# Kernel optimization log

Measured on AMD Instinct MI355X. Metric: run time of the kernel, lower is better.

Reference implementation:

```python
import jax, jax.numpy as jnp
import numpy as np

VOCAB, DIM, B, L, OUT = 100000, 50, 4096, 512, 20

def setup_inputs() -> dict:
    key = jax.random.key(0)
    k1, k2, k3, k4, k5 = jax.random.split(key, 5)
    x = jax.random.randint(k1, (B, L), 0, VOCAB, dtype=jnp.int64)
    lengths = jax.random.randint(k2, (B,), 1, L + 1, dtype=jnp.int64)  # at least 1 token
    emb_table = jax.random.normal(k3, (VOCAB, DIM), dtype=jnp.float32)
    W = jax.random.normal(k4, (OUT, DIM), dtype=jnp.float32) * 0.1
    b = jax.random.normal(k5, (OUT,), dtype=jnp.float32) * 0.1
    return {"x": x, "lengths": lengths, "emb_table": emb_table, "W": W, "b": b}

def reference(x, lengths, emb_table, W, b):
    # embedding gather: [B, L, D]
    emb = emb_table[x]
    # masked mean over the first lengths[i] tokens of each sample
    mask = (jnp.arange(emb.shape[1])[None, :] < lengths[:, None]).astype(emb.dtype)  # [B, L]
    denom = lengths.astype(emb.dtype)[:, None]                                        # [B, 1]
    rep = jnp.einsum('bld,bl->bd', emb, mask) / denom                                 # [B, D]
    rep = jax.nn.relu(rep)
    logits = rep @ W.T + b                                                            # [B, OUT]
    return logits
```

## Files before the change

kernel.cpp:

```cpp
#include <hip/hip_runtime.h>
#include <hip/hip_fp16.h>


#define LMAX    512
#define DIMV    50
#define OUTV    20
#define VOCABSZ 100000
#define RSTRIDE 64
#define NSHARD  8
#define SHROWS  12500
#define BINCAP  576
#define TABBLKS 3126

struct __align__(16) H8 { __half2 h[4]; };

#define OFF_GBIN  (16u << 20)
#define OFF_BOFS  (28u << 20)
#define OFF_PART  (29u << 20)

__device__ inline void accum(float4& a0, float4& a1, const H8& h) {
    float2 f0 = __half22float2(h.h[0]);
    float2 f1 = __half22float2(h.h[1]);
    float2 f2 = __half22float2(h.h[2]);
    float2 f3 = __half22float2(h.h[3]);
    a0.x += f0.x; a0.y += f0.y; a0.z += f1.x; a0.w += f1.y;
    a1.x += f2.x; a1.y += f2.y; a1.z += f3.x; a1.w += f3.y;
}

__global__ __launch_bounds__(256) void prep(
    const float* __restrict__ emb, const int* __restrict__ x,
    const int* __restrict__ lengths, char* __restrict__ ws)
{
    const int tid = threadIdx.x;

    if (blockIdx.x < TABBLKS) {
        __half* tab = (__half*)ws;
        const int t = blockIdx.x * 256 + tid;
        const int r = t >> 3, q = t & 7;
        if (r > VOCABSZ) return;
        float v[8] = {0.f,0.f,0.f,0.f,0.f,0.f,0.f,0.f};
        if (r < VOCABSZ) {
            const float* src = emb + r * DIMV + q * 8;
            if (q < 6) {
                #pragma unroll
                for (int j = 0; j < 8; j += 2) {
                    float2 a = *reinterpret_cast<const float2*>(src + j);
                    v[j] = a.x; v[j + 1] = a.y;
                }
            } else if (q == 6) {
                float2 a = *reinterpret_cast<const float2*>(src);
                v[0] = a.x; v[1] = a.y;
            }
        }
        H8 h;
        h.h[0] = __floats2half2_rn(v[0], v[1]);
        h.h[1] = __floats2half2_rn(v[2], v[3]);
        h.h[2] = __floats2half2_rn(v[4], v[5]);
        h.h[3] = __floats2half2_rn(v[6], v[7]);
        *reinterpret_cast<H8*>(tab + r * RSTRIDE + q * 8) = h;
        return;
    }

    const int b = blockIdx.x - TABBLKS;
    int*  gbin = (int*)(ws + OFF_GBIN);
    int2* bofs = (int2*)(ws + OFF_BOFS);

    __shared__ int sidx[LMAX];
    __shared__ int sbin[BINCAP];
    __shared__ int cnt[NSHARD], pcnt[NSHARD], base[NSHARD], pos[NSHARD];

    if (tid < NSHARD) { cnt[tid] = 0; pos[tid] = 0; }
    __syncthreads();

    const int len = lengths[b];
    #pragma unroll
    for (int i = tid; i < LMAX; i += 256) {
        const int v = x[b * LMAX + i];
        sidx[i] = v;
        if (i < len) atomicAdd(&cnt[v / SHROWS], 1);
    }
    __syncthreads();
    if (tid == 0) {
        int run = 0;
        #pragma unroll
        for (int s = 0; s < NSHARD; ++s) {
            base[s] = run;
            pcnt[s] = (cnt[s] + 7) & ~7;
            run += pcnt[s];
        }
    }
    __syncthreads();
    #pragma unroll
    for (int i = tid; i < LMAX; i += 256) {
        if (i < len) {
            const int v = sidx[i];
            const int s = v / SHROWS;
            const int p = atomicAdd(&pos[s], 1);
            sbin[base[s] + p] = v;
        }
    }
    __syncthreads();
    if (tid < 64) {
        const int s = tid >> 3, k = tid & 7;
        if (cnt[s] + k < pcnt[s]) sbin[base[s] + cnt[s] + k] = VOCABSZ;
    }
    __syncthreads();
    const int total = base[NSHARD - 1] + pcnt[NSHARD - 1];
    for (int j = tid; j < total; j += 256) gbin[b * BINCAP + j] = sbin[j];
    if (tid < NSHARD) bofs[b * NSHARD + tid] = make_int2(base[tid], pcnt[tid]);
}

__global__ __launch_bounds__(256) void shard_gather(char* __restrict__ ws)
{
    const __half* tab  = (const __half*)ws;
    const int*    gbin = (const int*)(ws + OFF_GBIN);
    const int2*   bofs = (const int2*)(ws + OFF_BOFS);
    float*        part = (float*)(ws + OFF_PART);

    const int s    = blockIdx.x & 7;
    const int grp  = blockIdx.x >> 3;
    const int tid  = threadIdx.x;
    const int wave = tid >> 6, lane = tid & 63;
    const int rg   = lane >> 3, cl = lane & 7;
    const int b    = grp * 4 + wave;

    __shared__ int slab[4][520];

    const int2 of = bofs[b * NSHARD + s];
    const int* seg = gbin + b * BINCAP + of.x;
    for (int i = lane; i < of.y; i += 64) slab[wave][i] = seg[i];
    __syncthreads();

    const __half* tabc = tab + cl * 8;
    const int nch = of.y >> 3;
    float4 a0 = {0.f,0.f,0.f,0.f}, a1 = {0.f,0.f,0.f,0.f};
    int c = 0;
    for (; c + 3 < nch; c += 4) {
        const int i0 = slab[wave][(c    ) * 8 + rg];
        const int i1 = slab[wave][(c + 1) * 8 + rg];
        const int i2 = slab[wave][(c + 2) * 8 + rg];
        const int i3 = slab[wave][(c + 3) * 8 + rg];
        H8 h0 = *reinterpret_cast<const H8*>(tabc + (i0 << 6));
        H8 h1 = *reinterpret_cast<const H8*>(tabc + (i1 << 6));
        H8 h2 = *reinterpret_cast<const H8*>(tabc + (i2 << 6));
        H8 h3 = *reinterpret_cast<const H8*>(tabc + (i3 << 6));
        accum(a0, a1, h0); accum(a0, a1, h1);
        accum(a0, a1, h2); accum(a0, a1, h3);
    }
    for (; c < nch; ++c) {
        const int i0 = slab[wave][c * 8 + rg];
        H8 h0 = *reinterpret_cast<const H8*>(tabc + (i0 << 6));
        accum(a0, a1, h0);
    }

    #pragma unroll
    for (int m = 8; m <= 32; m <<= 1) {
        a0.x += __shfl_xor(a0.x, m); a0.y += __shfl_xor(a0.y, m);
        a0.z += __shfl_xor(a0.z, m); a0.w += __shfl_xor(a0.w, m);
        a1.x += __shfl_xor(a1.x, m); a1.y += __shfl_xor(a1.y, m);
        a1.z += __shfl_xor(a1.z, m); a1.w += __shfl_xor(a1.w, m);
    }
    if (lane < 8) {
        float* p = part + b * (NSHARD * 64) + s * 64 + lane * 8;
        *reinterpret_cast<float4*>(p)     = a0;
        *reinterpret_cast<float4*>(p + 4) = a1;
    }
}

__global__ __launch_bounds__(256) void finalize(
    const int* __restrict__ lengths, const float* __restrict__ W,
    const float* __restrict__ bias, const char* __restrict__ ws,
    float* __restrict__ out)
{
    const float* part = (const float*)(ws + OFF_PART);
    const int tid = threadIdx.x, wave = tid >> 6, lane = tid & 63;
    const int b = blockIdx.x * 4 + wave;

    __shared__ float srep[4][64];

    float v = 0.f;
    #pragma unroll
    for (int s = 0; s < NSHARD; ++s)
        v += part[b * (NSHARD * 64) + s * 64 + lane];
    const float inv = 1.0f / (float)lengths[b];
    srep[wave][lane] = fmaxf(v * inv, 0.f);
    __syncthreads();

    if (lane < OUTV) {
        float acc = bias[lane];
        const float* wr = W + lane * DIMV;
        #pragma unroll
        for (int d = 0; d < DIMV; ++d) acc += srep[wave][d] * wr[d];
        out[b * OUTV + lane] = acc;
    }
}

__global__ __launch_bounds__(256) void fused_gather(
    const int*    __restrict__ x,
    const int*    __restrict__ lengths,
    const __half* __restrict__ tab,
    const float*  __restrict__ W,
    const float*  __restrict__ bias,
    float*        __restrict__ out)
{
    const int b    = blockIdx.x;
    const int tid  = threadIdx.x;
    const int wave = tid >> 6;
    const int lane = tid & 63;
    const int rg   = lane >> 3;
    const int cl   = lane & 7;

    __shared__ int   sidx[LMAX];
    __shared__ float sacc[4][64];
    __shared__ float srep[DIMV];

    const int len = lengths[b];
    const int xbase = b * LMAX;
    #pragma unroll
    for (int i = 0; i < LMAX; i += 256) {
        const int ii = i + tid;
        const int v  = x[xbase + ii];
        sidx[ii] = (ii < len) ? v : VOCABSZ;
    }
    __syncthreads();

    const __half* tabc = tab + cl * 8;
    const int nchunk = (len + 7) >> 3;
    float4 a0 = {0.f,0.f,0.f,0.f}, a1 = {0.f,0.f,0.f,0.f};

    int c = wave;
    for (; c + 28 < nchunk; c += 32) {
        int i0 = sidx[(c     ) * 8 + rg];
        int i1 = sidx[(c +  4) * 8 + rg];
        int i2 = sidx[(c +  8) * 8 + rg];
        int i3 = sidx[(c + 12) * 8 + rg];
        int i4 = sidx[(c + 16) * 8 + rg];
        int i5 = sidx[(c + 20) * 8 + rg];
        int i6 = sidx[(c + 24) * 8 + rg];
        int i7 = sidx[(c + 28) * 8 + rg];
        H8 h0 = *reinterpret_cast<const H8*>(tabc + (i0 << 6));
        H8 h1 = *reinterpret_cast<const H8*>(tabc + (i1 << 6));
        H8 h2 = *reinterpret_cast<const H8*>(tabc + (i2 << 6));
        H8 h3 = *reinterpret_cast<const H8*>(tabc + (i3 << 6));
        H8 h4 = *reinterpret_cast<const H8*>(tabc + (i4 << 6));
        H8 h5 = *reinterpret_cast<const H8*>(tabc + (i5 << 6));
        H8 h6 = *reinterpret_cast<const H8*>(tabc + (i6 << 6));
        H8 h7 = *reinterpret_cast<const H8*>(tabc + (i7 << 6));
        accum(a0, a1, h0); accum(a0, a1, h1); accum(a0, a1, h2); accum(a0, a1, h3);
        accum(a0, a1, h4); accum(a0, a1, h5); accum(a0, a1, h6); accum(a0, a1, h7);
    }
    for (; c < nchunk; c += 4) {
        int i0 = sidx[c * 8 + rg];
        H8 h0 = *reinterpret_cast<const H8*>(tabc + (i0 << 6));
        accum(a0, a1, h0);
    }

    #pragma unroll
    for (int m = 8; m <= 32; m <<= 1) {
        a0.x += __shfl_xor(a0.x, m); a0.y += __shfl_xor(a0.y, m);
        a0.z += __shfl_xor(a0.z, m); a0.w += __shfl_xor(a0.w, m);
        a1.x += __shfl_xor(a1.x, m); a1.y += __shfl_xor(a1.y, m);
        a1.z += __shfl_xor(a1.z, m); a1.w += __shfl_xor(a1.w, m);
    }
    if (lane < 8) {
        *reinterpret_cast<float4*>(&sacc[wave][lane * 8])     = a0;
        *reinterpret_cast<float4*>(&sacc[wave][lane * 8 + 4]) = a1;
    }
    __syncthreads();

    if (tid < DIMV) {
        float s = sacc[0][tid] + sacc[1][tid] + sacc[2][tid] + sacc[3][tid];
        srep[tid] = fmaxf(s / (float)len, 0.f);
    }
    __syncthreads();

    if (tid < OUTV) {
        float s = bias[tid];
        const float* wr = W + tid * DIMV;
        #pragma unroll
        for (int d = 0; d < DIMV; ++d) s += srep[d] * wr[d];
        out[b * OUTV + tid] = s;
    }
}

extern "C" void kernel_launch(void* const* d_in, const int* in_sizes, int n_in,
                              void* d_out, int out_size, void* d_ws, size_t ws_size,
                              hipStream_t stream) {
    const int*   x       = (const int*)  d_in[0];
    const int*   lengths = (const int*)  d_in[1];
    const float* emb     = (const float*)d_in[2];
    const float* W       = (const float*)d_in[3];
    const float* bias    = (const float*)d_in[4];
    float* out = (float*)d_out;
    char*  ws  = (char*)d_ws;

    const int B = in_sizes[1];
    const size_t NEED = (size_t)OFF_PART + (size_t)B * NSHARD * 64 * sizeof(float);

    if (ws_size >= NEED) {
        prep<<<TABBLKS + B, 256, 0, stream>>>(emb, x, lengths, ws);
        shard_gather<<<(B / 4) * NSHARD, 256, 0, stream>>>(ws);
        finalize<<<B / 4, 256, 0, stream>>>(lengths, W, bias, ws, out);
    } else {
        prep<<<TABBLKS, 256, 0, stream>>>(emb, x, lengths, ws);
        fused_gather<<<B, 256, 0, stream>>>(x, lengths, (const __half*)ws, W, bias, out);
    }
}
```

Baseline: 103.4 us.

## Use 16-bit shard-local indices, per-shard padded table, and atomic shard reduction

The fp16 table is laid out per shard, each shard padded with a zero row, so bins can store 16-bit local indices instead of 32-bit global ones. This halves the index traffic in bins and in LDS. Shard partial sums are now combined with float atomics into a single rep buffer that prep zeroes, instead of writing eight partial vectors and summing them in finalize. The small-workspace fused fallback is removed and the unneeded __syncthreads in shard_gather is dropped. In exchange, atomics add contention and make the summation order nondeterministic.

```diff
diff --git a/kernel.cpp b/kernel.cpp
--- a/kernel.cpp
+++ b/kernel.cpp
@@ -2,21 +2,22 @@
 #include <hip/hip_fp16.h>
 
 
-#define LMAX    512
-#define DIMV    50
-#define OUTV    20
-#define VOCABSZ 100000
-#define RSTRIDE 64
-#define NSHARD  8
-#define SHROWS  12500
-#define BINCAP  576
-#define TABBLKS 3126
+#define LMAX     512
+#define DIMV     50
+#define OUTV     20
+#define VOCABSZ  100000
+#define NSHARD   8
+#define SHROWS   12500
+#define SHSTRIDE 12501
+#define BINCAP   576
+#define NROWS8   (NSHARD * SHSTRIDE)
+#define TABBLKS  ((NROWS8 * 8 + 255) / 256)
 
 struct __align__(16) H8 { __half2 h[4]; };
 
-#define OFF_GBIN  (16u << 20)
-#define OFF_BOFS  (28u << 20)
-#define OFF_PART  (29u << 20)
+#define OFF_GBIN (16u << 20)
+#define OFF_BOFS (21u << 20)
+#define OFF_REP  (22u << 20)
 
 __device__ inline void accum(float4& a0, float4& a1, const H8& h) {
     float2 f0 = __half22float2(h.h[0]);
@@ -35,12 +36,15 @@
 
     if (blockIdx.x < TABBLKS) {
         __half* tab = (__half*)ws;
-        const int t = blockIdx.x * 256 + tid;
-        const int r = t >> 3, q = t & 7;
-        if (r > VOCABSZ) return;
+        const int t  = blockIdx.x * 256 + tid;
+        const int r8 = t >> 3, q = t & 7;
+        if (r8 >= NROWS8) return;
+        const int s     = r8 / SHSTRIDE;
+        const int local = r8 - s * SHSTRIDE;
         float v[8] = {0.f,0.f,0.f,0.f,0.f,0.f,0.f,0.f};
-        if (r < VOCABSZ) {
-            const float* src = emb + r * DIMV + q * 8;
+        if (local < SHROWS) {
+            const int vr = s * SHROWS + local;
+            const float* src = emb + vr * DIMV + q * 8;
             if (q < 6) {
                 #pragma unroll
                 for (int j = 0; j < 8; j += 2) {
@@ -57,19 +61,21 @@
         h.h[1] = __floats2half2_rn(v[2], v[3]);
         h.h[2] = __floats2half2_rn(v[4], v[5]);
         h.h[3] = __floats2half2_rn(v[6], v[7]);
-        *reinterpret_cast<H8*>(tab + r * RSTRIDE + q * 8) = h;
+        *reinterpret_cast<H8*>(tab + r8 * 64 + q * 8) = h;
         return;
     }
 
     const int b = blockIdx.x - TABBLKS;
-    int*  gbin = (int*)(ws + OFF_GBIN);
-    int2* bofs = (int2*)(ws + OFF_BOFS);
-
-    __shared__ int sidx[LMAX];
-    __shared__ int sbin[BINCAP];
+    ushort* gbin = (ushort*)(ws + OFF_GBIN);
+    int2*   bofs = (int2*)  (ws + OFF_BOFS);
+    float*  rep  = (float*) (ws + OFF_REP);
+
+    __shared__ int    sidx[LMAX];
+    __shared__ ushort sbin[BINCAP];
     __shared__ int cnt[NSHARD], pcnt[NSHARD], base[NSHARD], pos[NSHARD];
 
     if (tid < NSHARD) { cnt[tid] = 0; pos[tid] = 0; }
+    if (tid < 64) rep[b * 64 + tid] = 0.f;
     __syncthreads();
 
     const int len = lengths[b];
@@ -80,14 +86,11 @@
         if (i < len) atomicAdd(&cnt[v / SHROWS], 1);
     }
     __syncthreads();
-    if (tid == 0) {
+    if (tid < NSHARD) {
         int run = 0;
-        #pragma unroll
-        for (int s = 0; s < NSHARD; ++s) {
-            base[s] = run;
-            pcnt[s] = (cnt[s] + 7) & ~7;
-            run += pcnt[s];
-        }
+        for (int j = 0; j < tid; ++j) run += (cnt[j] + 7) & ~7;
+        base[tid] = run;
+        pcnt[tid] = (cnt[tid] + 7) & ~7;
     }
     __syncthreads();
     #pragma unroll
@@ -96,13 +99,13 @@
             const int v = sidx[i];
             const int s = v / SHROWS;
             const int p = atomicAdd(&pos[s], 1);
-            sbin[base[s] + p] = v;
+            sbin[base[s] + p] = (ushort)(v - s * SHROWS);
         }
     }
     __syncthreads();
     if (tid < 64) {
         const int s = tid >> 3, k = tid & 7;
-        if (cnt[s] + k < pcnt[s]) sbin[base[s] + cnt[s] + k] = VOCABSZ;
+        if (cnt[s] + k < pcnt[s]) sbin[base[s] + cnt[s] + k] = (ushort)SHROWS;
     }
     __syncthreads();
     const int total = base[NSHARD - 1] + pcnt[NSHARD - 1];
@@ -113,25 +116,24 @@
 __global__ __launch_bounds__(256) void shard_gather(char* __restrict__ ws)
 {
     const __half* tab  = (const __half*)ws;
-    const int*    gbin = (const int*)(ws + OFF_GBIN);
-    const int2*   bofs = (const int2*)(ws + OFF_BOFS);
-    float*        part = (float*)(ws + OFF_PART);
+    const ushort* gbin = (const ushort*)(ws + OFF_GBIN);
+    const int2*   bofs = (const int2*)  (ws + OFF_BOFS);
+    float*        rep  = (float*)       (ws + OFF_REP);
 
     const int s    = blockIdx.x & 7;
     const int grp  = blockIdx.x >> 3;
     const int tid  = threadIdx.x;
     const int wave = tid >> 6, lane = tid & 63;
     const int rg   = lane >> 3, cl = lane & 7;
-    const int b    = grp * 4 + wave;
-
-    __shared__ int slab[4][520];
-
+
+    __shared__ ushort slab[4][LMAX];
+
+    const int b  = grp * 4 + wave;
     const int2 of = bofs[b * NSHARD + s];
-    const int* seg = gbin + b * BINCAP + of.x;
+    const ushort* seg = gbin + b * BINCAP + of.x;
     for (int i = lane; i < of.y; i += 64) slab[wave][i] = seg[i];
-    __syncthreads();
-
-    const __half* tabc = tab + cl * 8;
+
+    const __half* tabs = tab + s * (SHSTRIDE * 64) + cl * 8;
     const int nch = of.y >> 3;
     float4 a0 = {0.f,0.f,0.f,0.f}, a1 = {0.f,0.f,0.f,0.f};
     int c = 0;
@@ -140,16 +142,16 @@
         const int i1 = slab[wave][(c + 1) * 8 + rg];
         const int i2 = slab[wave][(c + 2) * 8 + rg];
         const int i3 = slab[wave][(c + 3) * 8 + rg];
-        H8 h0 = *reinterpret_cast<const H8*>(tabc + (i0 << 6));
-        H8 h1 = *reinterpret_cast<const H8*>(tabc + (i1 << 6));
-        H8 h2 = *reinterpret_cast<const H8*>(tabc + (i2 << 6));
-        H8 h3 = *reinterpret_cast<const H8*>(tabc + (i3 << 6));
+        H8 h0 = *reinterpret_cast<const H8*>(tabs + (i0 << 6));
+        H8 h1 = *reinterpret_cast<const H8*>(tabs + (i1 << 6));
+        H8 h2 = *reinterpret_cast<const H8*>(tabs + (i2 << 6));
+        H8 h3 = *reinterpret_cast<const H8*>(tabs + (i3 << 6));
         accum(a0, a1, h0); accum(a0, a1, h1);
         accum(a0, a1, h2); accum(a0, a1, h3);
     }
     for (; c < nch; ++c) {
         const int i0 = slab[wave][c * 8 + rg];
-        H8 h0 = *reinterpret_cast<const H8*>(tabc + (i0 << 6));
+        H8 h0 = *reinterpret_cast<const H8*>(tabs + (i0 << 6));
         accum(a0, a1, h0);
     }
 
@@ -161,9 +163,11 @@
         a1.z += __shfl_xor(a1.z, m); a1.w += __shfl_xor(a1.w, m);
     }
     if (lane < 8) {
-        float* p = part + b * (NSHARD * 64) + s * 64 + lane * 8;
-        *reinterpret_cast<float4*>(p)     = a0;
-        *reinterpret_cast<float4*>(p + 4) = a1;
+        float* p = rep + b * 64 + lane * 8;
+        atomicAdd(p + 0, a0.x); atomicAdd(p + 1, a0.y);
+        atomicAdd(p + 2, a0.z); atomicAdd(p + 3, a0.w);
+        atomicAdd(p + 4, a1.x); atomicAdd(p + 5, a1.y);
+        atomicAdd(p + 6, a1.z); atomicAdd(p + 7, a1.w);
     }
 }
 
@@ -172,16 +176,13 @@
     const float* __restrict__ bias, const char* __restrict__ ws,
     float* __restrict__ out)
 {
-    const float* part = (const float*)(ws + OFF_PART);
+    const float* rep = (const float*)(ws + OFF_REP);
     const int tid = threadIdx.x, wave = tid >> 6, lane = tid & 63;
     const int b = blockIdx.x * 4 + wave;
 
     __shared__ float srep[4][64];
 
-    float v = 0.f;
-    #pragma unroll
-    for (int s = 0; s < NSHARD; ++s)
-        v += part[b * (NSHARD * 64) + s * 64 + lane];
+    const float v   = rep[b * 64 + lane];
     const float inv = 1.0f / (float)lengths[b];
     srep[wave][lane] = fmaxf(v * inv, 0.f);
     __syncthreads();
@@ -192,94 +193,6 @@
         #pragma unroll
         for (int d = 0; d < DIMV; ++d) acc += srep[wave][d] * wr[d];
         out[b * OUTV + lane] = acc;
-    }
-}
-
-__global__ __launch_bounds__(256) void fused_gather(
-    const int*    __restrict__ x,
-    const int*    __restrict__ lengths,
-    const __half* __restrict__ tab,
-    const float*  __restrict__ W,
-    const float*  __restrict__ bias,
-    float*        __restrict__ out)
-{
-    const int b    = blockIdx.x;
-    const int tid  = threadIdx.x;
-    const int wave = tid >> 6;
-    const int lane = tid & 63;
-    const int rg   = lane >> 3;
-    const int cl   = lane & 7;
-
-    __shared__ int   sidx[LMAX];
-    __shared__ float sacc[4][64];
-    __shared__ float srep[DIMV];
-
-    const int len = lengths[b];
-    const int xbase = b * LMAX;
-    #pragma unroll
-    for (int i = 0; i < LMAX; i += 256) {
-        const int ii = i + tid;
-        const int v  = x[xbase + ii];
-        sidx[ii] = (ii < len) ? v : VOCABSZ;
-    }
-    __syncthreads();
-
-    const __half* tabc = tab + cl * 8;
-    const int nchunk = (len + 7) >> 3;
-    float4 a0 = {0.f,0.f,0.f,0.f}, a1 = {0.f,0.f,0.f,0.f};
-
-    int c = wave;
-    for (; c + 28 < nchunk; c += 32) {
-        int i0 = sidx[(c     ) * 8 + rg];
-        int i1 = sidx[(c +  4) * 8 + rg];
-        int i2 = sidx[(c +  8) * 8 + rg];
-        int i3 = sidx[(c + 12) * 8 + rg];
-        int i4 = sidx[(c + 16) * 8 + rg];
-        int i5 = sidx[(c + 20) * 8 + rg];
-        int i6 = sidx[(c + 24) * 8 + rg];
-        int i7 = sidx[(c + 28) * 8 + rg];
-        H8 h0 = *reinterpret_cast<const H8*>(tabc + (i0 << 6));
-        H8 h1 = *reinterpret_cast<const H8*>(tabc + (i1 << 6));
-        H8 h2 = *reinterpret_cast<const H8*>(tabc + (i2 << 6));
-        H8 h3 = *reinterpret_cast<const H8*>(tabc + (i3 << 6));
-        H8 h4 = *reinterpret_cast<const H8*>(tabc + (i4 << 6));
-        H8 h5 = *reinterpret_cast<const H8*>(tabc + (i5 << 6));
-        H8 h6 = *reinterpret_cast<const H8*>(tabc + (i6 << 6));
-        H8 h7 = *reinterpret_cast<const H8*>(tabc + (i7 << 6));
-        accum(a0, a1, h0); accum(a0, a1, h1); accum(a0, a1, h2); accum(a0, a1, h3);
-        accum(a0, a1, h4); accum(a0, a1, h5); accum(a0, a1, h6); accum(a0, a1, h7);
-    }
-    for (; c < nchunk; c += 4) {
-        int i0 = sidx[c * 8 + rg];
-        H8 h0 = *reinterpret_cast<const H8*>(tabc + (i0 << 6));
-        accum(a0, a1, h0);
-    }
-
-    #pragma unroll
-    for (int m = 8; m <= 32; m <<= 1) {
-        a0.x += __shfl_xor(a0.x, m); a0.y += __shfl_xor(a0.y, m);
-        a0.z += __shfl_xor(a0.z, m); a0.w += __shfl_xor(a0.w, m);
-        a1.x += __shfl_xor(a1.x, m); a1.y += __shfl_xor(a1.y, m);
-        a1.z += __shfl_xor(a1.z, m); a1.w += __shfl_xor(a1.w, m);
-    }
-    if (lane < 8) {
-        *reinterpret_cast<float4*>(&sacc[wave][lane * 8])     = a0;
-        *reinterpret_cast<float4*>(&sacc[wave][lane * 8 + 4]) = a1;
-    }
-    __syncthreads();
-
-    if (tid < DIMV) {
-        float s = sacc[0][tid] + sacc[1][tid] + sacc[2][tid] + sacc[3][tid];
-        srep[tid] = fmaxf(s / (float)len, 0.f);
-    }
-    __syncthreads();
-
-    if (tid < OUTV) {
-        float s = bias[tid];
-        const float* wr = W + tid * DIMV;
-        #pragma unroll
-        for (int d = 0; d < DIMV; ++d) s += srep[d] * wr[d];
-        out[b * OUTV + tid] = s;
     }
 }
 
@@ -295,14 +208,8 @@
     char*  ws  = (char*)d_ws;
 
     const int B = in_sizes[1];
-    const size_t NEED = (size_t)OFF_PART + (size_t)B * NSHARD * 64 * sizeof(float);
-
-    if (ws_size >= NEED) {
-        prep<<<TABBLKS + B, 256, 0, stream>>>(emb, x, lengths, ws);
-        shard_gather<<<(B / 4) * NSHARD, 256, 0, stream>>>(ws);
-        finalize<<<B / 4, 256, 0, stream>>>(lengths, W, bias, ws, out);
-    } else {
-        prep<<<TABBLKS, 256, 0, stream>>>(emb, x, lengths, ws);
-        fused_gather<<<B, 256, 0, stream>>>(x, lengths, (const __half*)ws, W, bias, out);
-    }
-}
+
+    prep<<<TABBLKS + B, 256, 0, stream>>>(emb, x, lengths, ws);
+    shard_gather<<<(B / 4) * NSHARD, 256, 0, stream>>>(ws);
+    finalize<<<B / 4, 256, 0, stream>>>(lengths, W, bias, ws, out);
+}
```

Result: slower. 151.7 us (+46.6%).
